# Optimization experiments

Hardware: AMD Instinct MI355X
Metric: run time of the kernel (lower is better)

Reference implementation:

```python
import jax, jax.numpy as jnp
import numpy as np

N_SPECIES = 2
N_RBF = 16
HIDDEN = 64
CUTOFF = 2.5


def setup_inputs() -> dict:
    key = jax.random.key(0)
    ks = jax.random.split(key, 10)
    B, N = 8, 1024
    positions = jax.random.uniform(ks[0], (B, N, 3), dtype=jnp.float32) * 10.0
    types = jax.random.randint(ks[1], (B, N), 0, N_SPECIES)
    in_dim = N_SPECIES + N_SPECIES * N_RBF  # 34
    def lin(k, fan_in, fan_out):
        bound = 1.0 / np.sqrt(fan_in)
        kw, kb = jax.random.split(k)
        W = jax.random.uniform(kw, (fan_in, fan_out), minval=-bound, maxval=bound, dtype=jnp.float32)
        b = jax.random.uniform(kb, (fan_out,), minval=-bound, maxval=bound, dtype=jnp.float32)
        return W, b
    W1, b1 = lin(ks[2], in_dim, 64)
    W2, b2 = lin(ks[3], 64, 64)
    W3, b3 = lin(ks[4], 64, HIDDEN)
    return {"positions": positions, "types": types,
            "W1": W1, "b1": b1, "W2": W2, "b2": b2, "W3": W3, "b3": b3}


def _forward(positions, types, W1, b1, W2, b2, W3, b3):
    B, N, _ = positions.shape
    # pairwise distances with safe sqrt (zero grad on diagonal, matching torch norm subgradient)
    disp = positions[:, :, None, :] - positions[:, None, :, :]          # [B,N,N,3]
    sq = jnp.sum(disp * disp, axis=-1)                                   # [B,N,N]
    nz = sq > 0.0
    d = jnp.sqrt(jnp.where(nz, sq, 1.0)) * nz
    # RBF expansion
    centers = jnp.linspace(0.0, CUTOFF, N_RBF)
    widths = jnp.full((N_RBF,), CUTOFF / max(N_RBF - 1, 1))
    diff = d[..., None] - centers                                        # [B,N,N,R]
    rbf = jnp.exp(-(diff ** 2) / (widths ** 2 + 1e-12))
    # smooth polynomial cutoff
    x = d / CUTOFF
    cut = jnp.where(d < CUTOFF, 1.0 - 6.0 * x ** 5 + 15.0 * x ** 4 - 10.0 * x ** 3, 0.0)
    rbf = rbf * cut[..., None]
    eye = jnp.eye(N, dtype=bool)[None, :, :, None]
    rbf = jnp.where(eye, 0.0, rbf)
    # species-weighted neighbor aggregation
    onehot = jax.nn.one_hot(types, N_SPECIES, dtype=positions.dtype)      # [B,N,S]
    env = jnp.einsum('bijr,bjs->birs', rbf, onehot).reshape(B, N, -1)     # [B,N,R*S]
    feats = jnp.concatenate([onehot, env], axis=-1)                       # [B,N,S+S*R]
    h = jax.nn.silu(feats @ W1 + b1)
    h = jax.nn.silu(h @ W2 + b2)
    return h @ W3 + b3                                                    # [B,N,HIDDEN]


def reference(positions, types, W1, b1, W2, b2, W3, b3):
    return _forward(positions, types, W1, b1, W2, b2, W3, b3)
```

## Files before the change

kernel.cpp:

```cpp
#include <hip/hip_runtime.h>
#include <hip/hip_bf16.h>

#define NTHREADS 256
#define N_ATOMS 1024
#define HIDDEN 64

__global__ __launch_bounds__(NTHREADS) void LocalFeatureEncoder_40063454937486_kernel(
    const float* __restrict__ pos,
    const int*   __restrict__ types,
    const float* __restrict__ W1,
    const float* __restrict__ b1,
    const float* __restrict__ W2,
    const float* __restrict__ b2,
    const float* __restrict__ W3,
    const float* __restrict__ b3,
    float*       __restrict__ out)
{
    const int a    = blockIdx.x;
    const int bidx = a >> 10;
    const int i    = a & (N_ATOMS - 1);
    const int tid  = threadIdx.x;
    const int lane = tid & 63;
    const int wav  = tid >> 6;

    __shared__ float qd [N_ATOMS];
    __shared__ float qm0[N_ATOMS];
    __shared__ float qm1[N_ATOMS];
    __shared__ float partial[4 * 32];
    __shared__ float feats[64];
    __shared__ float h1s[64];
    __shared__ int   cnt;

    const float* pf   = pos + (size_t)bidx * (N_ATOMS * 3);
    const int*   typb = types + (size_t)bidx * N_ATOMS;

    const float4 p0 = *(const float4*)(pf + tid * 12);
    const float4 p1 = *(const float4*)(pf + tid * 12 + 4);
    const float4 p2 = *(const float4*)(pf + tid * 12 + 8);
    const int4   tv = *(const int4*)(typb + tid * 4);

    const float xi = pf[i * 3 + 0];
    const float yi = pf[i * 3 + 1];
    const float zi = pf[i * 3 + 2];

    if (tid == 0) cnt = 0;
    __syncthreads();

    {
        const float px[4] = {p0.x, p0.w, p1.z, p2.y};
        const float py[4] = {p0.y, p1.x, p1.w, p2.z};
        const float pz[4] = {p0.z, p1.y, p2.x, p2.w};
        const int   tj[4] = {tv.x, tv.y, tv.z, tv.w};

#pragma unroll
        for (int q = 0; q < 4; ++q) {
            const int j = tid * 4 + q;
            const float dx = xi - px[q], dy = yi - py[q], dz = zi - pz[q];
            const float sq = dx * dx + dy * dy + dz * dz;
            const bool pred = (j != i) && (sq < 6.25f);

            const unsigned long long mask = __ballot(pred);
            int base = 0;
            if (lane == 0 && mask) base = atomicAdd(&cnt, (int)__popcll(mask));
            base = __shfl(base, 0, 64);
            if (pred) {
                const float d  = sqrtf(sq);
                const float x  = d * 0.4f;
                const float x3 = x * x * x;
                const float cutv = 1.0f + x3 * (-10.0f + x * (15.0f - 6.0f * x));
                const int idx = base + (int)__popcll(mask & ((1ull << lane) - 1ull));
                qd [idx] = d;
                qm0[idx] = (tj[q] == 0) ? cutv : 0.0f;
                qm1[idx] = (tj[q] == 0) ? 0.0f : cutv;
            }
        }
    }
    __syncthreads();
    const int n = cnt;

    {
        const int p = tid >> 5;
        const int f = tid & 31;
        const int r = f >> 1;
        const int s = f & 1;
        const float c = (float)r * (2.5f / 15.0f);
        const float inv_w2 = 36.0f;
        const float* __restrict__ qm = (s == 0) ? qm0 : qm1;

        float acc = 0.0f;
        for (int e = p; e < n; e += 8) {
            const float d    = qd[e];
            const float m    = qm[e];
            const float diff = d - c;
            acc += m * __expf(-(diff * diff) * inv_w2);
        }
        acc += __shfl_xor(acc, 32, 64);
        if (lane < 32) partial[wav * 32 + f] = acc;
        if (tid == 0) {
            const int ti = typb[i];
            feats[0] = (ti == 0) ? 1.0f : 0.0f;
            feats[1] = (ti == 1) ? 1.0f : 0.0f;
        }
    }
    __syncthreads();
    if (tid < 32)
        feats[2 + tid] = partial[tid] + partial[32 + tid] + partial[64 + tid] + partial[96 + tid];
    __syncthreads();

    if (tid < HIDDEN) {
        float h = b1[tid];
#pragma unroll
        for (int k = 0; k < 34; k++) h += feats[k] * W1[k * HIDDEN + tid];
        h = h / (1.0f + __expf(-h));
        h1s[tid] = h;
    }
    __syncthreads();
    if (tid < HIDDEN) {
        float h = b2[tid];
#pragma unroll
        for (int k = 0; k < HIDDEN; k++) h += h1s[k] * W2[k * HIDDEN + tid];
        h = h / (1.0f + __expf(-h));
        feats[tid] = h;
    }
    __syncthreads();
    if (tid < HIDDEN) {
        float o = b3[tid];
#pragma unroll
        for (int k = 0; k < HIDDEN; k++) o += feats[k] * W3[k * HIDDEN + tid];
        out[(size_t)a * HIDDEN + tid] = o;
    }
}

extern "C" void kernel_launch(void* const* d_in, const int* in_sizes, int n_in,
                              void* d_out, int out_size, void* d_ws, size_t ws_size,
                              hipStream_t stream) {
    const float* pos   = (const float*)d_in[0];
    const int*   types = (const int*)d_in[1];
    const float* W1    = (const float*)d_in[2];
    const float* b1    = (const float*)d_in[3];
    const float* W2    = (const float*)d_in[4];
    const float* b2    = (const float*)d_in[5];
    const float* W3    = (const float*)d_in[6];
    const float* b3    = (const float*)d_in[7];
    float*       out   = (float*)d_out;

    const int BN = in_sizes[1];

    LocalFeatureEncoder_40063454937486_kernel<<<BN, NTHREADS, 0, stream>>>(
        pos, types, W1, b1, W2, b2, W3, b3, out);
}
```

Before: 89.01 us.

## Use per-wave neighbor lists and share one exp across both species

Each wave now compacts its in-cutoff neighbors into its own shared-memory segment, which replaces the block-wide atomic counter and drops one barrier. Each entry is packed as a float2 of distance and a species-signed cutoff weight. Each thread then handles one RBF center and evaluates the Gaussian once per neighbor, accumulating both species channels from the sign of the weight. This halves the exp count and the LDS reads, at the cost of padding each segment to a multiple of 16 and looping over four segments.

```diff
diff --git a/kernel.cpp b/kernel.cpp
--- a/kernel.cpp
+++ b/kernel.cpp
@@ -2,8 +2,9 @@
 #include <hip/hip_bf16.h>
 
 #define NTHREADS 256
-#define N_ATOMS 1024
-#define HIDDEN 64
+#define N_ATOMS  1024
+#define HIDDEN   64
+#define SEGCAP   272
 
 __global__ __launch_bounds__(NTHREADS) void LocalFeatureEncoder_40063454937486_kernel(
     const float* __restrict__ pos,
@@ -23,13 +24,12 @@
     const int lane = tid & 63;
     const int wav  = tid >> 6;
 
-    __shared__ float qd [N_ATOMS];
-    __shared__ float qm0[N_ATOMS];
-    __shared__ float qm1[N_ATOMS];
-    __shared__ float partial[4 * 32];
-    __shared__ float feats[64];
-    __shared__ float h1s[64];
-    __shared__ int   cnt;
+    __shared__ float2 qdm[4 * SEGCAP];
+    __shared__ float2 part2[4 * 16];
+    __shared__ int    nseg[4];
+    __shared__ float  feats[64];
+    __shared__ float  h1s[64];
+    __shared__ float  h2s[64];
 
     const float* pf   = pos + (size_t)bidx * (N_ATOMS * 3);
     const int*   typb = types + (size_t)bidx * N_ATOMS;
@@ -43,14 +43,13 @@
     const float yi = pf[i * 3 + 1];
     const float zi = pf[i * 3 + 2];
 
-    if (tid == 0) cnt = 0;
-    __syncthreads();
-
     {
         const float px[4] = {p0.x, p0.w, p1.z, p2.y};
         const float py[4] = {p0.y, p1.x, p1.w, p2.z};
         const float pz[4] = {p0.z, p1.y, p2.x, p2.w};
         const int   tj[4] = {tv.x, tv.y, tv.z, tv.w};
+        float2* seg = &qdm[wav * SEGCAP];
+        int base = 0;
 
 #pragma unroll
         for (int q = 0; q < 4; ++q) {
@@ -60,51 +59,61 @@
             const bool pred = (j != i) && (sq < 6.25f);
 
             const unsigned long long mask = __ballot(pred);
-            int base = 0;
-            if (lane == 0 && mask) base = atomicAdd(&cnt, (int)__popcll(mask));
-            base = __shfl(base, 0, 64);
             if (pred) {
                 const float d  = sqrtf(sq);
                 const float x  = d * 0.4f;
                 const float x3 = x * x * x;
                 const float cutv = 1.0f + x3 * (-10.0f + x * (15.0f - 6.0f * x));
                 const int idx = base + (int)__popcll(mask & ((1ull << lane) - 1ull));
-                qd [idx] = d;
-                qm0[idx] = (tj[q] == 0) ? cutv : 0.0f;
-                qm1[idx] = (tj[q] == 0) ? 0.0f : cutv;
+                seg[idx] = make_float2(d, (tj[q] == 0) ? cutv : -cutv);
+            }
+            base += (int)__popcll(mask);
+        }
+        const int npad = (base + 15) & ~15;
+        if (lane < npad - base) seg[base + lane] = make_float2(0.0f, 0.0f);
+        if (lane == 0) nseg[wav] = npad;
+    }
+    __syncthreads();
+
+    {
+        const int   p = tid >> 4;
+        const int   r = tid & 15;
+        const float c = (float)r * (2.5f / 15.0f);
+
+        float acc0 = 0.0f, acc1 = 0.0f;
+#pragma unroll
+        for (int w = 0; w < 4; ++w) {
+            const int n = nseg[w];
+            const float2* s = &qdm[w * SEGCAP];
+            for (int e = p; e < n; e += 16) {
+                const float2 dm  = s[e];
+                const float diff = dm.x - c;
+                const float ex   = __expf(diff * diff * -36.0f);
+                acc0 += ex * fmaxf(dm.y, 0.0f);
+                acc1 += ex * fmaxf(-dm.y, 0.0f);
             }
         }
+        acc0 += __shfl_xor(acc0, 16, 64);
+        acc0 += __shfl_xor(acc0, 32, 64);
+        acc1 += __shfl_xor(acc1, 16, 64);
+        acc1 += __shfl_xor(acc1, 32, 64);
+        if (lane < 16) part2[wav * 16 + lane] = make_float2(acc0, acc1);
     }
     __syncthreads();
-    const int n = cnt;
 
-    {
-        const int p = tid >> 5;
-        const int f = tid & 31;
-        const int r = f >> 1;
-        const int s = f & 1;
-        const float c = (float)r * (2.5f / 15.0f);
-        const float inv_w2 = 36.0f;
-        const float* __restrict__ qm = (s == 0) ? qm0 : qm1;
-
-        float acc = 0.0f;
-        for (int e = p; e < n; e += 8) {
-            const float d    = qd[e];
-            const float m    = qm[e];
-            const float diff = d - c;
-            acc += m * __expf(-(diff * diff) * inv_w2);
-        }
-        acc += __shfl_xor(acc, 32, 64);
-        if (lane < 32) partial[wav * 32 + f] = acc;
-        if (tid == 0) {
-            const int ti = typb[i];
-            feats[0] = (ti == 0) ? 1.0f : 0.0f;
-            feats[1] = (ti == 1) ? 1.0f : 0.0f;
-        }
+    if (tid < 16) {
+        const float2 a0 = part2[tid];
+        const float2 a1 = part2[16 + tid];
+        const float2 a2 = part2[32 + tid];
+        const float2 a3 = part2[48 + tid];
+        feats[2 + 2 * tid + 0] = a0.x + a1.x + a2.x + a3.x;
+        feats[2 + 2 * tid + 1] = a0.y + a1.y + a2.y + a3.y;
     }
-    __syncthreads();
-    if (tid < 32)
-        feats[2 + tid] = partial[tid] + partial[32 + tid] + partial[64 + tid] + partial[96 + tid];
+    if (tid == 16) {
+        const int ti = typb[i];
+        feats[0] = (ti == 0) ? 1.0f : 0.0f;
+        feats[1] = (ti == 1) ? 1.0f : 0.0f;
+    }
     __syncthreads();
 
     if (tid < HIDDEN) {
@@ -120,13 +129,13 @@
 #pragma unroll
         for (int k = 0; k < HIDDEN; k++) h += h1s[k] * W2[k * HIDDEN + tid];
         h = h / (1.0f + __expf(-h));
-        feats[tid] = h;
+        h2s[tid] = h;
     }
     __syncthreads();
     if (tid < HIDDEN) {
         float o = b3[tid];
 #pragma unroll
-        for (int k = 0; k < HIDDEN; k++) o += feats[k] * W3[k * HIDDEN + tid];
+        for (int k = 0; k < HIDDEN; k++) o += h2s[k] * W3[k * HIDDEN + tid];
         out[(size_t)a * HIDDEN + tid] = o;
     }
 }
```

After: 89.34 us. About the same (+0.4%).
